# Kernel tuning notes

Hardware: AMD Instinct MI355X
Metric: run time of the kernel (lower is better)

## Reference

```python
import jax, jax.numpy as jnp
import numpy as np

N = 200000   # active voxels
K = 27       # 3x3x3 kernel volume
CIN = 32
COUT = 64


def setup_inputs() -> dict:
    key = jax.random.key(0)
    k1, k2, k3, k4 = jax.random.split(key, 4)
    features = jax.random.normal(k1, (N, CIN), dtype=jnp.float32)
    # kernel map: for each kernel offset k and output voxel n, index of the
    # contributing input voxel (or masked out if that neighbor is inactive)
    neighbor_map = jax.random.randint(k2, (K, N), 0, N, dtype=jnp.int32)
    neighbor_mask = jax.random.randint(k3, (K, N), 0, 2) > 0
    std = 1.0 / float(np.sqrt(CIN * K))  # matches reset_parameters
    kernel = jax.random.uniform(k4, (K, CIN, COUT), dtype=jnp.float32,
                                minval=-std, maxval=std)
    return {"features": features, "neighbor_map": neighbor_map,
            "neighbor_mask": neighbor_mask, "kernel": kernel}


def reference(features, neighbor_map, neighbor_mask, kernel):
    # Sparse conv3d as gather -> per-offset matmul -> accumulate.
    # scan over the K=27 kernel offsets keeps peak memory at one gathered
    # [N, CIN] buffer instead of materializing [K, N, CIN].
    n_out = features.shape[0]
    cout = kernel.shape[-1]

    def body(acc, inp):
        nm_k, mask_k, w_k = inp  # [N], [N], [CIN, COUT]
        g = features[nm_k] * mask_k[:, None].astype(features.dtype)  # gather [N, CIN]
        return acc + g @ w_k, None

    init = jnp.zeros((n_out, cout), dtype=features.dtype)
    out, _ = jax.lax.scan(body, init, (neighbor_map, neighbor_mask, kernel))
    return out
```

## Files before the change

### kernel.cpp

```cpp
#include <hip/hip_runtime.h>

#define CIN   32
#define COUT  64
#define K_OFF 27

typedef __attribute__((ext_vector_type(8))) short bf16x8;
typedef __attribute__((ext_vector_type(4))) float f32x4;

__device__ inline unsigned short f2bf_rne(float f) {
    union { float f; unsigned int u; } v; v.f = f;
    unsigned int u = v.u;
    u = (u + 0x7fffu + ((u >> 16) & 1u)) >> 16;
    return (unsigned short)u;
}

__global__ __launch_bounds__(256) void detect_mask(
    const unsigned char* __restrict__ mask, int nbytes, int* __restrict__ flag) {
    __shared__ int wany[4];
    int found = 0;
    for (int i = threadIdx.x; i < nbytes; i += 256)
        if ((i & 3) && mask[i]) found = 1;
    unsigned long long b = __ballot(found);
    if ((threadIdx.x & 63) == 0) wany[threadIdx.x >> 6] = b ? 1 : 0;
    __syncthreads();
    if (threadIdx.x == 0) *flag = wany[0] | wany[1] | wany[2] | wany[3];
}

__global__ __launch_bounds__(256) void prep_kernel(
    const float* __restrict__ feat, const float* __restrict__ wk,
    unsigned short* __restrict__ featb, unsigned short* __restrict__ wt2,
    int n, int Bf)
{
    const int gid = blockIdx.x;
    if (gid < Bf) {
        const int base = (gid * 256 + threadIdx.x) * 8;
        if (base < n * CIN) {
            float4 a = *(const float4*)(feat + base);
            float4 b = *(const float4*)(feat + base + 4);
            bf16x8 v;
            v[0] = (short)f2bf_rne(a.x); v[1] = (short)f2bf_rne(a.y);
            v[2] = (short)f2bf_rne(a.z); v[3] = (short)f2bf_rne(a.w);
            v[4] = (short)f2bf_rne(b.x); v[5] = (short)f2bf_rne(b.y);
            v[6] = (short)f2bf_rne(b.z); v[7] = (short)f2bf_rne(b.w);
            *(bf16x8*)(featb + base) = v;
        }
    } else {
        const int t = (gid - Bf) * 256 + threadIdx.x;
        if (t < K_OFF * 4 * 64) {
            const int lane = t & 63, ct = (t >> 6) & 3, k = t >> 8;
            const int lrow = lane & 15, q = lane >> 4;
            const int col = ct * 16 + lrow;
            bf16x8 v;
            #pragma unroll
            for (int j = 0; j < 8; ++j)
                v[j] = (short)f2bf_rne(wk[(k * CIN + q * 8 + j) * COUT + col]);
            *(bf16x8*)(wt2 + t * 8) = v;
        }
    }
}

__global__ __launch_bounds__(256) void conv_mfma3(
    const unsigned short* __restrict__ featb,
    const int*            __restrict__ nmap,
    const unsigned char*  __restrict__ maskb,
    const unsigned short* __restrict__ wt2,
    float* __restrict__ out, int n, const int* __restrict__ flag)
{
    const int tid  = threadIdx.x;
    const int wave = tid >> 6;
    const int lane = tid & 63;
    const int lrow = lane & 15;
    const int q    = lane >> 4;
    const int n0w  = blockIdx.x * 256 + wave * 64;
    const int mshift = (*flag) ? 0 : 2;

    const int  myrow  = n0w + lane;
    const bool rvalid = myrow < n;

    auto load_mi = [&](int k) -> int {
        if (!rvalid) return -1;
        const int idx = k * n + myrow;
        const unsigned char mv = maskb[(size_t)idx << mshift];
        const int nm = nmap[idx];
        return mv ? nm : -1;
    };
    auto do_gathers = [&](int mi_raw, bf16x8* dst) {
        #pragma unroll
        for (int rt = 0; rt < 4; ++rt) {
            const int mi = __shfl(mi_raw, rt * 16 + lrow);
            bf16x8 v = {0, 0, 0, 0, 0, 0, 0, 0};
            if (mi >= 0) v = *(const bf16x8*)(featb + (size_t)mi * CIN + q * 8);
            dst[rt] = v;
        }
    };
    auto loadB = [&](int k, bf16x8* dst) {
        const unsigned short* p = wt2 + ((k * 4) << 9) + lane * 8;
        #pragma unroll
        for (int ct = 0; ct < 4; ++ct) dst[ct] = *(const bf16x8*)(p + (ct << 9));
    };

    int    mi_buf[2];
    bf16x8 a_buf[3][4];
    bf16x8 B_buf[2][4];
    f32x4  acc[4][4] = {};

    {
        const int m0 = load_mi(0);
        const int m1 = load_mi(1);
        mi_buf[0] = load_mi(2);
        loadB(0, B_buf[0]);
        do_gathers(m0, a_buf[0]);
        do_gathers(m1, a_buf[1]);
    }

    #pragma unroll
    for (int k = 0; k < K_OFF; ++k) {
        if (k + 3 < K_OFF) mi_buf[(k + 1) & 1] = load_mi(k + 3);
        if (k + 2 < K_OFF) do_gathers(mi_buf[k & 1], a_buf[(k + 2) % 3]);
        if (k + 1 < K_OFF) loadB(k + 1, B_buf[(k + 1) & 1]);

        const int s = k % 3, bs = k & 1;
        #pragma unroll
        for (int rt = 0; rt < 4; ++rt)
            #pragma unroll
            for (int ct = 0; ct < 4; ++ct)
                acc[rt][ct] = __builtin_amdgcn_mfma_f32_16x16x32_bf16(
                    a_buf[s][rt], B_buf[bs][ct], acc[rt][ct], 0, 0, 0);
    }

    #pragma unroll
    for (int rt = 0; rt < 4; ++rt)
        #pragma unroll
        for (int ct = 0; ct < 4; ++ct)
            #pragma unroll
            for (int r = 0; r < 4; ++r) {
                const int row = n0w + rt * 16 + q * 4 + r;
                if (row < n) out[(size_t)row * COUT + ct * 16 + lrow] = acc[rt][ct][r];
            }
}

#define BN 64
__global__ __launch_bounds__(256) void sparse_conv_fp32(
    const float* __restrict__ feat, const int* __restrict__ nmap,
    const unsigned char* __restrict__ mask8, const int* __restrict__ mask32,
    const float* __restrict__ wk, float* __restrict__ out,
    int n, const int* __restrict__ flag)
{
    __shared__ float A[CIN][BN];
    __shared__ float W[CIN][COUT];
    const int tid = threadIdx.x;
    const int n0 = blockIdx.x * BN;
    const int is_b8 = *flag;
    const int r0 = (tid >> 4) * 4, c0 = (tid & 15) * 4;
    const int grow = tid >> 2, gpart = tid & 3;
    float acc[4][4] = {};
    for (int k = 0; k < K_OFF; ++k) {
        {
            const int base = tid * 8;
            const float* wsrc = wk + (size_t)k * (CIN * COUT) + base;
            float4 w0 = ((const float4*)wsrc)[0];
            float4 w1 = ((const float4*)wsrc)[1];
            *(float4*)&W[base >> 6][base & 63] = w0;
            *(float4*)&W[base >> 6][(base & 63) + 4] = w1;
        }
        {
            const int gn = n0 + grow;
            float4 f0 = make_float4(0.f, 0.f, 0.f, 0.f), f1 = f0;
            if (gn < n) {
                const int idx = k * n + gn;
                const int m = is_b8 ? (int)mask8[idx] : mask32[idx];
                if (m) {
                    const float* fsrc = feat + (size_t)nmap[idx] * CIN + gpart * 8;
                    f0 = ((const float4*)fsrc)[0];
                    f1 = ((const float4*)fsrc)[1];
                }
            }
            const int cb = gpart * 8;
            A[cb+0][grow]=f0.x; A[cb+1][grow]=f0.y; A[cb+2][grow]=f0.z; A[cb+3][grow]=f0.w;
            A[cb+4][grow]=f1.x; A[cb+5][grow]=f1.y; A[cb+6][grow]=f1.z; A[cb+7][grow]=f1.w;
        }
        __syncthreads();
        #pragma unroll
        for (int c = 0; c < CIN; ++c) {
            const float4 a = *(const float4*)&A[c][r0];
            const float4 w = *(const float4*)&W[c][c0];
            acc[0][0]+=a.x*w.x; acc[0][1]+=a.x*w.y; acc[0][2]+=a.x*w.z; acc[0][3]+=a.x*w.w;
            acc[1][0]+=a.y*w.x; acc[1][1]+=a.y*w.y; acc[1][2]+=a.y*w.z; acc[1][3]+=a.y*w.w;
            acc[2][0]+=a.z*w.x; acc[2][1]+=a.z*w.y; acc[2][2]+=a.z*w.z; acc[2][3]+=a.z*w.w;
            acc[3][0]+=a.w*w.x; acc[3][1]+=a.w*w.y; acc[3][2]+=a.w*w.z; acc[3][3]+=a.w*w.w;
        }
        __syncthreads();
    }
    #pragma unroll
    for (int i = 0; i < 4; ++i) {
        const int orow = n0 + r0 + i;
        if (orow < n)
            *(float4*)&out[(size_t)orow * COUT + c0] =
                make_float4(acc[i][0], acc[i][1], acc[i][2], acc[i][3]);
    }
}

static inline size_t align16(size_t x) { return (x + 15) & ~(size_t)15; }

extern "C" void kernel_launch(void* const* d_in, const int* in_sizes, int n_in,
                              void* d_out, int out_size, void* d_ws, size_t ws_size,
                              hipStream_t stream) {
    const float*         feat = (const float*)d_in[0];
    const int*           nmap = (const int*)d_in[1];
    const unsigned char* m8   = (const unsigned char*)d_in[2];
    const int*           m32  = (const int*)d_in[2];
    const float*         wk   = (const float*)d_in[3];
    float*               out  = (float*)d_out;

    const int n = in_sizes[0] / CIN;
    int* flag = (int*)d_ws;

    const size_t feat_off   = 128;
    const size_t feat_bytes = (size_t)n * CIN * 2;
    const size_t wt2_off    = align16(feat_off + feat_bytes);
    const size_t wt2_bytes  = (size_t)K_OFF * 4 * 64 * 8 * 2;
    const size_t needed     = wt2_off + wt2_bytes;

    const int mask_elems = K_OFF * n;
    const int det_bytes  = mask_elems < 4096 ? mask_elems : 4096;
    detect_mask<<<1, 256, 0, stream>>>(m8, det_bytes, flag);

    if (ws_size >= needed) {
        unsigned short* featb = (unsigned short*)((char*)d_ws + feat_off);
        unsigned short* wt2   = (unsigned short*)((char*)d_ws + wt2_off);
        const int Bf = (n * CIN / 8 + 255) / 256;
        const int Bw = (K_OFF * 4 * 64 + 255) / 256;
        prep_kernel<<<Bf + Bw, 256, 0, stream>>>(feat, wk, featb, wt2, n, Bf);
        const int nblocks = (n + 255) / 256;
        conv_mfma3<<<nblocks, 256, 0, stream>>>(featb, nmap, m8, wt2, out, n, flag);
    } else {
        const int nb = (n + BN - 1) / BN;
        sparse_conv_fp32<<<nb, 256, 0, stream>>>(feat, nmap, m8, m32, wk, out, n, flag);
    }
}
```

Before: 183.0 us.

## Fold mask detection into prep kernel and halve rows per wave in MFMA conv

```diff
diff --git a/kernel.cpp b/kernel.cpp
--- a/kernel.cpp
+++ b/kernel.cpp
@@ -14,22 +14,11 @@
     return (unsigned short)u;
 }
 
-__global__ __launch_bounds__(256) void detect_mask(
-    const unsigned char* __restrict__ mask, int nbytes, int* __restrict__ flag) {
-    __shared__ int wany[4];
-    int found = 0;
-    for (int i = threadIdx.x; i < nbytes; i += 256)
-        if ((i & 3) && mask[i]) found = 1;
-    unsigned long long b = __ballot(found);
-    if ((threadIdx.x & 63) == 0) wany[threadIdx.x >> 6] = b ? 1 : 0;
-    __syncthreads();
-    if (threadIdx.x == 0) *flag = wany[0] | wany[1] | wany[2] | wany[3];
-}
-
 __global__ __launch_bounds__(256) void prep_kernel(
     const float* __restrict__ feat, const float* __restrict__ wk,
+    const unsigned char* __restrict__ maskb,
     unsigned short* __restrict__ featb, unsigned short* __restrict__ wt2,
-    int n, int Bf)
+    int* __restrict__ flag, int n, int Bf, int Bw, int det_bytes)
 {
     const int gid = blockIdx.x;
     if (gid < Bf) {
@@ -44,7 +33,7 @@
             v[6] = (short)f2bf_rne(b.z); v[7] = (short)f2bf_rne(b.w);
             *(bf16x8*)(featb + base) = v;
         }
-    } else {
+    } else if (gid < Bf + Bw) {
         const int t = (gid - Bf) * 256 + threadIdx.x;
         if (t < K_OFF * 4 * 64) {
             const int lane = t & 63, ct = (t >> 6) & 3, k = t >> 8;
@@ -56,10 +45,19 @@
                 v[j] = (short)f2bf_rne(wk[(k * CIN + q * 8 + j) * COUT + col]);
             *(bf16x8*)(wt2 + t * 8) = v;
         }
-    }
-}
-
-__global__ __launch_bounds__(256) void conv_mfma3(
+    } else {
+        __shared__ int wany[4];
+        int found = 0;
+        for (int i = threadIdx.x; i < det_bytes; i += 256)
+            if ((i & 3) && maskb[i]) found = 1;
+        unsigned long long b = __ballot(found);
+        if ((threadIdx.x & 63) == 0) wany[threadIdx.x >> 6] = b ? 1 : 0;
+        __syncthreads();
+        if (threadIdx.x == 0) *flag = wany[0] | wany[1] | wany[2] | wany[3];
+    }
+}
+
+__global__ __launch_bounds__(256, 4) void conv_mfma6(
     const unsigned short* __restrict__ featb,
     const int*            __restrict__ nmap,
     const unsigned char*  __restrict__ maskb,
@@ -71,27 +69,25 @@
     const int lane = tid & 63;
     const int lrow = lane & 15;
     const int q    = lane >> 4;
-    const int n0w  = blockIdx.x * 256 + wave * 64;
+    const int n0   = blockIdx.x * 128 + wave * 32;
     const int mshift = (*flag) ? 0 : 2;
 
-    const int  myrow  = n0w + lane;
-    const bool rvalid = myrow < n;
-
-    auto load_mi = [&](int k) -> int {
-        if (!rvalid) return -1;
-        const int idx = k * n + myrow;
+    const int  row0 = n0 + lrow, row1 = n0 + 16 + lrow;
+    const bool vr0 = row0 < n, vr1 = row1 < n;
+
+    auto load_mi = [&](int k, int rt) -> int {
+        const int  r = rt ? row1 : row0;
+        const bool v = rt ? vr1 : vr0;
+        if (!v) return -1;
+        const int idx = k * n + r;
         const unsigned char mv = maskb[(size_t)idx << mshift];
         const int nm = nmap[idx];
         return mv ? nm : -1;
     };
-    auto do_gathers = [&](int mi_raw, bf16x8* dst) {
-        #pragma unroll
-        for (int rt = 0; rt < 4; ++rt) {
-            const int mi = __shfl(mi_raw, rt * 16 + lrow);
-            bf16x8 v = {0, 0, 0, 0, 0, 0, 0, 0};
-            if (mi >= 0) v = *(const bf16x8*)(featb + (size_t)mi * CIN + q * 8);
-            dst[rt] = v;
-        }
+    auto gather = [&](int mi) -> bf16x8 {
+        bf16x8 z = {0, 0, 0, 0, 0, 0, 0, 0};
+        if (mi >= 0) z = *(const bf16x8*)(featb + (size_t)mi * CIN + q * 8);
+        return z;
     };
     auto loadB = [&](int k, bf16x8* dst) {
         const unsigned short* p = wt2 + ((k * 4) << 9) + lane * 8;
@@ -99,44 +95,64 @@
         for (int ct = 0; ct < 4; ++ct) dst[ct] = *(const bf16x8*)(p + (ct << 9));
     };
 
-    int    mi_buf[2];
-    bf16x8 a_buf[3][4];
+    int    mi_buf[2][2];
+    bf16x8 a_buf[3][2];
     bf16x8 B_buf[2][4];
-    f32x4  acc[4][4] = {};
+    f32x4  acc[2][4] = {};
 
     {
-        const int m0 = load_mi(0);
-        const int m1 = load_mi(1);
-        mi_buf[0] = load_mi(2);
+        int t0 = load_mi(0, 0), t1 = load_mi(0, 1);
+        int u0 = load_mi(1, 0), u1 = load_mi(1, 1);
+        mi_buf[0][0] = load_mi(2, 0);
+        mi_buf[0][1] = load_mi(2, 1);
         loadB(0, B_buf[0]);
-        do_gathers(m0, a_buf[0]);
-        do_gathers(m1, a_buf[1]);
+        a_buf[0][0] = gather(t0); a_buf[0][1] = gather(t1);
+        a_buf[1][0] = gather(u0); a_buf[1][1] = gather(u1);
     }
 
     #pragma unroll
     for (int k = 0; k < K_OFF; ++k) {
-        if (k + 3 < K_OFF) mi_buf[(k + 1) & 1] = load_mi(k + 3);
-        if (k + 2 < K_OFF) do_gathers(mi_buf[k & 1], a_buf[(k + 2) % 3]);
+        if (k + 3 < K_OFF) {
+            mi_buf[(k + 1) & 1][0] = load_mi(k + 3, 0);
+            mi_buf[(k + 1) & 1][1] = load_mi(k + 3, 1);
+        }
+        if (k + 2 < K_OFF) {
+            a_buf[(k + 2) % 3][0] = gather(mi_buf[k & 1][0]);
+            a_buf[(k + 2) % 3][1] = gather(mi_buf[k & 1][1]);
+        }
         if (k + 1 < K_OFF) loadB(k + 1, B_buf[(k + 1) & 1]);
 
         const int s = k % 3, bs = k & 1;
         #pragma unroll
-        for (int rt = 0; rt < 4; ++rt)
-            #pragma unroll
-            for (int ct = 0; ct < 4; ++ct)
-                acc[rt][ct] = __builtin_amdgcn_mfma_f32_16x16x32_bf16(
-                    a_buf[s][rt], B_buf[bs][ct], acc[rt][ct], 0, 0, 0);
+        for (int ct = 0; ct < 4; ++ct) {
+            acc[0][ct] = __builtin_amdgcn_mfma_f32_16x16x32_bf16(
+                a_buf[s][0], B_buf[bs][ct], acc[0][ct], 0, 0, 0);
+            acc[1][ct] = __builtin_amdgcn_mfma_f32_16x16x32_bf16(
+                a_buf[s][1], B_buf[bs][ct], acc[1][ct], 0, 0, 0);
+        }
     }
 
     #pragma unroll
-    for (int rt = 0; rt < 4; ++rt)
+    for (int rt = 0; rt < 2; ++rt)
         #pragma unroll
         for (int ct = 0; ct < 4; ++ct)
             #pragma unroll
             for (int r = 0; r < 4; ++r) {
-                const int row = n0w + rt * 16 + q * 4 + r;
+                const int row = n0 + rt * 16 + q * 4 + r;
                 if (row < n) out[(size_t)row * COUT + ct * 16 + lrow] = acc[rt][ct][r];
             }
+}
+
+__global__ __launch_bounds__(256) void detect_mask(
+    const unsigned char* __restrict__ mask, int nbytes, int* __restrict__ flag) {
+    __shared__ int wany[4];
+    int found = 0;
+    for (int i = threadIdx.x; i < nbytes; i += 256)
+        if ((i & 3) && mask[i]) found = 1;
+    unsigned long long b = __ballot(found);
+    if ((threadIdx.x & 63) == 0) wany[threadIdx.x >> 6] = b ? 1 : 0;
+    __syncthreads();
+    if (threadIdx.x == 0) *flag = wany[0] | wany[1] | wany[2] | wany[3];
 }
 
 #define BN 64
@@ -223,17 +239,18 @@
 
     const int mask_elems = K_OFF * n;
     const int det_bytes  = mask_elems < 4096 ? mask_elems : 4096;
-    detect_mask<<<1, 256, 0, stream>>>(m8, det_bytes, flag);
 
     if (ws_size >= needed) {
         unsigned short* featb = (unsigned short*)((char*)d_ws + feat_off);
         unsigned short* wt2   = (unsigned short*)((char*)d_ws + wt2_off);
         const int Bf = (n * CIN / 8 + 255) / 256;
         const int Bw = (K_OFF * 4 * 64 + 255) / 256;
-        prep_kernel<<<Bf + Bw, 256, 0, stream>>>(feat, wk, featb, wt2, n, Bf);
-        const int nblocks = (n + 255) / 256;
-        conv_mfma3<<<nblocks, 256, 0, stream>>>(featb, nmap, m8, wt2, out, n, flag);
+        prep_kernel<<<Bf + Bw + 1, 256, 0, stream>>>(
+            feat, wk, m8, featb, wt2, flag, n, Bf, Bw, det_bytes);
+        const int nblocks = (n + 127) / 128;
+        conv_mfma6<<<nblocks, 256, 0, stream>>>(featb, nmap, m8, wt2, out, n, flag);
     } else {
+        detect_mask<<<1, 256, 0, stream>>>(m8, det_bytes, flag);
         const int nb = (n + BN - 1) / BN;
         sparse_conv_fp32<<<nb, 256, 0, stream>>>(feat, nmap, m8, m32, wk, out, n, flag);
     }
```

Result: slower. 197.6 us (+8.0%).
